# Kernel optimization log

Hardware: AMD Instinct MI355X
Metric: run time of the kernel (lower is better)

The kernel has to match this reference:

```python
import jax, jax.numpy as jnp
import numpy as np
from jax import lax

EMBED_DIM = 128
N_RELATIONS = 64
N_ENTITIES = 100000
N_EDGES = 600000


def setup_inputs() -> dict:
    key = jax.random.key(0)
    k1, k2, k3, k4, k5, k6 = jax.random.split(key, 6)
    entity_emb = jax.random.normal(k1, (N_ENTITIES, EMBED_DIM), dtype=jnp.float32)
    heads = jax.random.randint(k2, (N_EDGES,), 0, N_ENTITIES)
    rels = jax.random.randint(k3, (N_EDGES,), 0, N_RELATIONS)
    tails = jax.random.randint(k4, (N_EDGES,), 0, N_ENTITIES)
    # learned params: relation embedding table (std=0.01) and square Linear weight (xavier)
    rel_embed_weight = 0.01 * jax.random.normal(k5, (N_RELATIONS, EMBED_DIM), dtype=jnp.float32)
    xavier = float(np.sqrt(6.0 / (EMBED_DIM + EMBED_DIM)))
    W = jax.random.uniform(k6, (EMBED_DIM, EMBED_DIM), dtype=jnp.float32, minval=-xavier, maxval=xavier)
    return {"entity_emb": entity_emb, "rel_embed_weight": rel_embed_weight, "W": W,
            "heads": heads, "rels": rels, "tails": tails}


def reference(entity_emb, rel_embed_weight, W, heads, rels, tails):
    n_entities = entity_emb.shape[0]
    # gather edge endpoint / relation embeddings: [E, D]
    e_h = entity_emb[heads]
    e_t = entity_emb[tails]
    e_r = rel_embed_weight[rels]
    # tanh-gated dot-product score per edge: [E]
    score = jnp.sum(e_t * jnp.tanh(e_h + e_r), axis=-1)
    # global max-shift (detached in torch) then per-head segment softmax
    score_exp = jnp.exp(score - lax.stop_gradient(jnp.max(score)))
    score_sum = jax.ops.segment_sum(score_exp, heads, num_segments=n_entities)
    attn = score_exp / (score_sum[heads] + 1e-10)
    # scatter-add attention-weighted messages back to head nodes: [N, D]
    agg = jax.ops.segment_sum(attn[:, None] * e_t, heads, num_segments=n_entities)
    # final Linear (no bias) + LeakyReLU(0.2); dropout is identity in eval mode
    out = (entity_emb + agg) @ W.T
    return jax.nn.leaky_relu(out, negative_slope=0.2)
```

## Files before the change

### kernel.cpp

```cpp
#include <hip/hip_runtime.h>
#include <math.h>

#define EMBED 128
#define BMAX 8192
#define LDSPAD 136
#define DBINS 64

#define TWO_LOG2E 2.8853900817779268f
#define DEFER_THR 32.0f

#define TMASK 0xFFFFF

typedef __attribute__((ext_vector_type(8))) short short8;
typedef __attribute__((ext_vector_type(4))) float floatx4;

__device__ __forceinline__ float ex2(float x) { return __builtin_amdgcn_exp2f(x); }

__device__ __forceinline__ float fast_tanh2(float x) {
    float e = ex2(TWO_LOG2E * x);
    return 1.0f - 2.0f * __builtin_amdgcn_rcpf(1.0f + e);
}

__device__ __forceinline__ unsigned short f2b(float f) {
    union { float f; unsigned int u; } v; v.f = f;
    unsigned int r = v.u + 0x7FFFu + ((v.u >> 16) & 1u);
    return (unsigned short)(r >> 16);
}

__device__ __forceinline__ float b2f(short u) {
    union { float f; unsigned int i; } v;
    v.i = ((unsigned int)(unsigned short)u) << 16;
    return v.f;
}

template <int CTRL>
__device__ __forceinline__ float dpp_add_f(float x) {
    int y = __builtin_amdgcn_update_dpp(0, __float_as_int(x), CTRL, 0xF, 0xF, false);
    return x + __int_as_float(y);
}
__device__ __forceinline__ float dpp_sum16(float s) {
    s = dpp_add_f<0x121>(s);
    s = dpp_add_f<0x122>(s);
    s = dpp_add_f<0x124>(s);
    s = dpp_add_f<0x128>(s);
    return s;
}

__global__ __launch_bounds__(256) void k_cast_hist(
    const float* __restrict__ ent, const float* __restrict__ rel, const float* __restrict__ W,
    short* __restrict__ entb, short* __restrict__ relb, short* __restrict__ wb,
    const int* __restrict__ heads, int* __restrict__ cnt, int* __restrict__ ghist,
    int ngE, int ngR, int ngW, int E)
{
    if (blockIdx.x == 0 && threadIdx.x < DBINS) ghist[threadIdx.x] = 0;
    int stride = gridDim.x * 256;
    int total = ngE + ngR + ngW;
    for (int g = blockIdx.x * 256 + threadIdx.x; g < total; g += stride) {
        const float4* src; short* dst;
        if (g < ngE)            { src = (const float4*)ent + (size_t)g * 2;              dst = entb + (size_t)g * 8; }
        else if (g < ngE + ngR) { int g2 = g - ngE;       src = (const float4*)rel + (size_t)g2 * 2; dst = relb + (size_t)g2 * 8; }
        else                    { int g2 = g - ngE - ngR; src = (const float4*)W   + (size_t)g2 * 2; dst = wb   + (size_t)g2 * 8; }
        float4 a = src[0], b = src[1];
        short8 o;
        o[0] = (short)f2b(a.x); o[1] = (short)f2b(a.y); o[2] = (short)f2b(a.z); o[3] = (short)f2b(a.w);
        o[4] = (short)f2b(b.x); o[5] = (short)f2b(b.y); o[6] = (short)f2b(b.z); o[7] = (short)f2b(b.w);
        *(short8*)dst = o;
    }
    for (int e = blockIdx.x * 256 + threadIdx.x; e < E; e += stride)
        atomicAdd(cnt + heads[e], 1);
}

__global__ __launch_bounds__(1024) void k_scan1(
    const int* __restrict__ cnt, int* __restrict__ offs,
    int* __restrict__ bsum, int* __restrict__ ghist, int N)
{
    __shared__ int wsum[16];
    __shared__ int dh[DBINS];
    const int tid = threadIdx.x;
    if (tid < DBINS) dh[tid] = 0;
    int i = blockIdx.x * 1024 + tid;
    int v = (i < N) ? cnt[i] : 0;
    __syncthreads();
    if (i < N) atomicAdd(&dh[v < DBINS ? v : DBINS - 1], 1);
    int x = v;
    #pragma unroll
    for (int d = 1; d < 64; d <<= 1) {
        int y = __shfl_up(x, d, 64);
        if ((tid & 63) >= d) x += y;
    }
    if ((tid & 63) == 63) wsum[tid >> 6] = x;
    __syncthreads();
    if (tid < 16) {
        int w = wsum[tid];
        #pragma unroll
        for (int d = 1; d < 16; d <<= 1) {
            int y = __shfl_up(w, d, 16);
            if (tid >= d) w += y;
        }
        wsum[tid] = w;
    }
    __syncthreads();
    int add = (tid >= 64) ? wsum[(tid >> 6) - 1] : 0;
    int incl = x + add;
    if (i < N) offs[i] = incl - v;
    if (tid == 1023) bsum[blockIdx.x] = incl;
    if (tid < DBINS && dh[tid] > 0) atomicAdd(ghist + tid, dh[tid]);
}

__global__ __launch_bounds__(256) void k_scan23(
    int* __restrict__ offs, const int* __restrict__ bsum,
    int* __restrict__ cursor, const int* __restrict__ cnt,
    const int* __restrict__ ghist, int* __restrict__ bincur,
    int* __restrict__ order, int N, int nb)
{
    __shared__ int sb[256];
    __shared__ int ws4[4];
    __shared__ int dbs[DBINS];
    __shared__ int lcnt[DBINS];
    __shared__ int lbase[DBINS];
    const int tid = threadIdx.x;

    int v = (tid < nb) ? bsum[tid] : 0;
    int x = v;
    #pragma unroll
    for (int d = 1; d < 64; d <<= 1) {
        int y = __shfl_up(x, d, 64);
        if ((tid & 63) >= d) x += y;
    }
    if ((tid & 63) == 63) ws4[tid >> 6] = x;
    __syncthreads();
    if (tid < 4) {
        int w = ws4[tid];
        #pragma unroll
        for (int d = 1; d < 4; d <<= 1) {
            int y = __shfl_up(w, d, 4);
            if (tid >= d) w += y;
        }
        ws4[tid] = w;
    }
    __syncthreads();
    int add = (tid >= 64) ? ws4[(tid >> 6) - 1] : 0;
    sb[tid] = x + add - v;

    if (tid < 64) {
        int g = ghist[tid];
        int s = g;
        #pragma unroll
        for (int d = 1; d < 64; d <<= 1) {
            int y = __shfl_up(s, d, 64);
            if (tid >= d) s += y;
        }
        dbs[tid] = s - g;
    }
    if (tid < DBINS) lcnt[tid] = 0;
    __syncthreads();

    int i = blockIdx.x * 256 + tid;
    int deg = 0, lrank = 0;
    if (i < N) {
        int o = offs[i] + sb[i >> 10];
        offs[i] = o;
        cursor[i] = o;
        int c = cnt[i];
        deg = c < DBINS ? c : DBINS - 1;
        lrank = atomicAdd(&lcnt[deg], 1);
    }
    __syncthreads();
    if (tid < DBINS) {
        int n = lcnt[tid];
        lbase[tid] = (n > 0) ? (dbs[tid] + atomicAdd(bincur + tid, n)) : 0;
    }
    __syncthreads();
    if (i < N) order[lbase[deg] + lrank] = i;
}

__global__ __launch_bounds__(256) void k_csr(
    const int* __restrict__ heads, const int* __restrict__ rels,
    const int* __restrict__ tails, int* __restrict__ cursor,
    int* __restrict__ trp, int E)
{
    int e = blockIdx.x * 256 + threadIdx.x;
    if (e >= E) return;
    int pos = atomicAdd(cursor + heads[e], 1);
    trp[pos] = tails[e] | (rels[e] << 20);
}

__global__ __launch_bounds__(256) void k_fused(
    const short* __restrict__ entb, const short* __restrict__ relb,
    const int* __restrict__ offs, const int* __restrict__ cnt,
    const int* __restrict__ trp, const int* __restrict__ order,
    short* __restrict__ accb, float* __restrict__ mh, float* __restrict__ lh,
    float* __restrict__ blockmax, int N, int R)
{
    const int tid = threadIdx.x;
    const int lane = tid & 15;
    int head0 = blockIdx.x * 16 + (tid >> 4);
    int head  = (head0 < N) ? order[(N - 1) - head0] : N;
    float mt = -INFINITY;
    if (head < N) {
        int start = offs[head];
        int c     = cnt[head];
        short8 hh = *((const short8*)(entb + (size_t)head * EMBED) + lane);
        float hf[8];
        #pragma unroll
        for (int i = 0; i < 8; ++i) hf[i] = b2f(hh[i]);
        float m = -INFINITY;
        float l = 0.f;
        float acc[8] = {0,0,0,0,0,0,0,0};
        for (int base = 0; base < c; base += 16) {
            int rem = c - base;
            int mm  = rem < 16 ? rem : 16;
            int trv = 0;
            if (lane < mm) trv = trp[start + base + lane];
            int p0 = __shfl(trv, 0, 16);
            short8 vtc = *((const short8*)(entb + (size_t)(p0 & TMASK) * EMBED) + lane);
            short8 vrc = *((const short8*)(relb + (size_t)(p0 >> 20) * EMBED) + lane);
            for (int j = 0; j < mm; ++j) {
                int jn = (j + 1 < mm) ? j + 1 : j;
                int pn = __shfl(trv, jn, 16);
                short8 vtn = *((const short8*)(entb + (size_t)(pn & TMASK) * EMBED) + lane);
                short8 vrn = *((const short8*)(relb + (size_t)(pn >> 20) * EMBED) + lane);
                float s = 0.f;
                float vtf[8];
                #pragma unroll
                for (int i = 0; i < 8; ++i) {
                    vtf[i] = b2f(vtc[i]);
                    s = fmaf(vtf[i], fast_tanh2(hf[i] + b2f(vrc[i])), s);
                }
                s = dpp_sum16(s);
                mt = fmaxf(mt, s);
                float dlt = s - m;
                if (dlt > DEFER_THR) {
                    float alpha = __expf(-dlt);
                    l *= alpha;
                    #pragma unroll
                    for (int q = 0; q < 8; ++q) acc[q] *= alpha;
                    m = s;
                    dlt = 0.f;
                }
                float p = __expf(dlt);
                l += p;
                #pragma unroll
                for (int q = 0; q < 8; ++q)
                    acc[q] = fmaf(p, vtf[q], acc[q]);
                vtc = vtn;
                vrc = vrn;
            }
        }
        short8 o;
        #pragma unroll
        for (int q = 0; q < 8; ++q) o[q] = (short)f2b(acc[q]);
        *((short8*)(accb + (size_t)head * EMBED) + lane) = o;
        if (lane == 0) { mh[head] = m; lh[head] = l; }
    }
    __shared__ float wmax[4];
    float wm = mt;
    #pragma unroll
    for (int off = 1; off < 64; off <<= 1) wm = fmaxf(wm, __shfl_xor(wm, off, 64));
    if ((tid & 63) == 0) wmax[tid >> 6] = wm;
    __syncthreads();
    if (tid == 0)
        blockmax[blockIdx.x] = fmaxf(fmaxf(wmax[0], wmax[1]), fmaxf(wmax[2], wmax[3]));
}

__global__ __launch_bounds__(256) void k_maxred(
    const float* __restrict__ blockmax, float* __restrict__ Mout, int n)
{
    __shared__ float smax[256];
    float m = -INFINITY;
    for (int i = threadIdx.x; i < n; i += 256) m = fmaxf(m, blockmax[i]);
    smax[threadIdx.x] = m;
    __syncthreads();
    for (int off = 128; off > 0; off >>= 1) {
        if ((int)threadIdx.x < off)
            smax[threadIdx.x] = fmaxf(smax[threadIdx.x], smax[threadIdx.x + off]);
        __syncthreads();
    }
    if (threadIdx.x == 0) Mout[0] = smax[0];
}

__global__ __launch_bounds__(256) void k_gemm_f(
    const short* __restrict__ entb, const short* __restrict__ accb,
    const float* __restrict__ mh, const float* __restrict__ lh,
    const float* __restrict__ Mptr, const short* __restrict__ wb,
    float* __restrict__ out, int N)
{
    __shared__ short xs[128 * LDSPAD];
    __shared__ short ws[128 * LDSPAD];
    __shared__ float invs[128];
    const int tid = threadIdx.x;
    const int n0  = blockIdx.x * 128;
    const float M = Mptr[0];

    if (tid < 128) {
        int g = n0 + tid;
        invs[tid] = (g < N) ? 1.0f / (lh[g] + 1e-10f * __expf(M - mh[g])) : 0.f;
    }
    #pragma unroll
    for (int it = 0; it < 8; ++it) {
        int ch = it * 256 + tid;
        int row = ch >> 4, col8 = ch & 15;
        *(short8*)(ws + row * LDSPAD + col8 * 8) = ((const short8*)wb)[ch];
    }
    __syncthreads();
    #pragma unroll
    for (int it = 0; it < 8; ++it) {
        int ch = it * 256 + tid;
        int row = ch >> 4, col8 = ch & 15;
        int g = n0 + row;
        short8 v = {0,0,0,0,0,0,0,0};
        if (g < N) {
            float inv = invs[row];
            short8 e8 = *((const short8*)(entb + (size_t)g * EMBED) + col8);
            short8 a8 = *((const short8*)(accb + (size_t)g * EMBED) + col8);
            #pragma unroll
            for (int q = 0; q < 8; ++q)
                v[q] = (short)f2b(b2f(e8[q]) + b2f(a8[q]) * inv);
        }
        *(short8*)(xs + row * LDSPAD + col8 * 8) = v;
    }
    __syncthreads();

    const int wv   = tid >> 6;
    const int lane = tid & 63;
    const int n16  = lane & 15;
    const int quad = lane >> 4;

    floatx4 acc[2][8];
    #pragma unroll
    for (int rt = 0; rt < 2; ++rt)
        #pragma unroll
        for (int jt = 0; jt < 8; ++jt)
            acc[rt][jt] = (floatx4){0.f, 0.f, 0.f, 0.f};

    #pragma unroll
    for (int kc = 0; kc < 4; ++kc) {
        int koff = kc * 32 + quad * 8;
        short8 a0 = *(const short8*)(xs + (wv * 32      + n16) * LDSPAD + koff);
        short8 a1 = *(const short8*)(xs + (wv * 32 + 16 + n16) * LDSPAD + koff);
        #pragma unroll
        for (int jt = 0; jt < 8; ++jt) {
            short8 b = *(const short8*)(ws + (jt * 16 + n16) * LDSPAD + koff);
            acc[0][jt] = __builtin_amdgcn_mfma_f32_16x16x32_bf16(a0, b, acc[0][jt], 0, 0, 0);
            acc[1][jt] = __builtin_amdgcn_mfma_f32_16x16x32_bf16(a1, b, acc[1][jt], 0, 0, 0);
        }
    }

    #pragma unroll
    for (int rt = 0; rt < 2; ++rt) {
        int rowbase = n0 + wv * 32 + rt * 16 + quad * 4;
        #pragma unroll
        for (int r = 0; r < 4; ++r) {
            int grow = rowbase + r;
            if (grow < N) {
                float* o = out + (size_t)grow * EMBED + n16;
                #pragma unroll
                for (int jt = 0; jt < 8; ++jt) {
                    float v = acc[rt][jt][r];
                    o[jt * 16] = (v > 0.f) ? v : 0.2f * v;
                }
            }
        }
    }
}

extern "C" void kernel_launch(void* const* d_in, const int* in_sizes, int n_in,
                              void* d_out, int out_size, void* d_ws, size_t ws_size,
                              hipStream_t stream)
{
    const float* ent   = (const float*)d_in[0];
    const float* rel   = (const float*)d_in[1];
    const float* W     = (const float*)d_in[2];
    const int*   heads = (const int*)d_in[3];
    const int*   rels  = (const int*)d_in[4];
    const int*   tails = (const int*)d_in[5];
    const int E = in_sizes[3];
    const int N = in_sizes[0] / EMBED;
    const int R = in_sizes[1] / EMBED;
    float* out = (float*)d_out;

    short* accb     = (short*)d_ws;
    float* mh       = (float*)(accb + (size_t)N * EMBED);
    float* lh       = mh + N;
    int*   trp      = (int*)(lh + N);
    int*   cnt      = trp + E;
    int*   bincur   = cnt + N;
    int*   offs     = bincur + DBINS;
    int*   cursor   = offs + N;
    float* blockmax = (float*)(cursor + N);
    float* Mval     = blockmax + BMAX;
    int*   bsum     = (int*)(Mval + 4);
    int*   ghist    = bsum + 1024;
    int*   order    = ghist + DBINS;
    short* wb       = (short*)(order + N);
    short* entb     = wb + 16384;
    short* relb     = entb + (size_t)N * EMBED;

    const int nb  = (N + 1023) >> 10;
    const int ngh = (N + 15) / 16;

    hipMemsetAsync(cnt, 0, (size_t)(N + DBINS) * sizeof(int), stream);

    int ngE = N * EMBED / 8, ngR = R * EMBED / 8, ngW = EMBED * EMBED / 8;
    k_cast_hist<<<2048, 256, 0, stream>>>(ent, rel, W, entb, relb, wb, heads, cnt, ghist, ngE, ngR, ngW, E);
    k_scan1<<<nb, 1024, 0, stream>>>(cnt, offs, bsum, ghist, N);
    k_scan23<<<(N + 255) / 256, 256, 0, stream>>>(offs, bsum, cursor, cnt, ghist, bincur, order, N, nb);
    k_csr<<<(E + 255) / 256, 256, 0, stream>>>(heads, rels, tails, cursor, trp, E);
    k_fused<<<ngh, 256, 0, stream>>>(entb, relb, offs, cnt, trp, order, accb, mh, lh, blockmax, N, R);
    k_maxred<<<1, 256, 0, stream>>>(blockmax, Mval, ngh);
    k_gemm_f<<<(N + 127) / 128, 256, 0, stream>>>(entb, accb, mh, lh, Mval, wb, out, N);
}
```

Baseline: 242.9 us.

## Fold global max reduction into fused kernel and load GEMM A operand directly

Removes the separate single-block max-reduction kernel: each k_fused block atomically bumps a done counter, and the last block to finish reduces all block maxima and writes the global max. The counter is zeroed by extending the existing memset. In k_gemm_f, the X tile is no longer staged through LDS; each lane loads its entity and aggregate rows from global memory, combines them, and feeds them straight into the MFMA. This cuts LDS use and a barrier, at the cost of uncoalesced 16-byte global reads per lane and a serial tail in the last fused block.

After: 462.7 us. 90.5% more time.

```diff
diff --git a/kernel.cpp b/kernel.cpp
--- a/kernel.cpp
+++ b/kernel.cpp
@@ -190,7 +190,8 @@
     const int* __restrict__ offs, const int* __restrict__ cnt,
     const int* __restrict__ trp, const int* __restrict__ order,
     short* __restrict__ accb, float* __restrict__ mh, float* __restrict__ lh,
-    float* __restrict__ blockmax, int N, int R)
+    float* __restrict__ blockmax, unsigned int* __restrict__ done,
+    float* __restrict__ Mout, int N, int R)
 {
     const int tid = threadIdx.x;
     const int lane = tid & 15;
@@ -254,29 +255,31 @@
         if (lane == 0) { mh[head] = m; lh[head] = l; }
     }
     __shared__ float wmax[4];
+    __shared__ int lastflag;
     float wm = mt;
     #pragma unroll
     for (int off = 1; off < 64; off <<= 1) wm = fmaxf(wm, __shfl_xor(wm, off, 64));
     if ((tid & 63) == 0) wmax[tid >> 6] = wm;
     __syncthreads();
-    if (tid == 0)
+    if (tid == 0) {
         blockmax[blockIdx.x] = fmaxf(fmaxf(wmax[0], wmax[1]), fmaxf(wmax[2], wmax[3]));
-}
-
-__global__ __launch_bounds__(256) void k_maxred(
-    const float* __restrict__ blockmax, float* __restrict__ Mout, int n)
-{
-    __shared__ float smax[256];
-    float m = -INFINITY;
-    for (int i = threadIdx.x; i < n; i += 256) m = fmaxf(m, blockmax[i]);
-    smax[threadIdx.x] = m;
-    __syncthreads();
-    for (int off = 128; off > 0; off >>= 1) {
-        if ((int)threadIdx.x < off)
-            smax[threadIdx.x] = fmaxf(smax[threadIdx.x], smax[threadIdx.x + off]);
+        __threadfence();
+        unsigned int prev = atomicAdd(done, 1u);
+        lastflag = (prev == gridDim.x - 1) ? 1 : 0;
+    }
+    __syncthreads();
+    if (lastflag) {
+        __threadfence();
+        const volatile float* bm = (const volatile float*)blockmax;
+        float m2 = -INFINITY;
+        for (int i = tid; i < (int)gridDim.x; i += 256) m2 = fmaxf(m2, bm[i]);
+        #pragma unroll
+        for (int off = 1; off < 64; off <<= 1) m2 = fmaxf(m2, __shfl_xor(m2, off, 64));
+        if ((tid & 63) == 0) wmax[tid >> 6] = m2;
         __syncthreads();
-    }
-    if (threadIdx.x == 0) Mout[0] = smax[0];
+        if (tid == 0)
+            Mout[0] = fmaxf(fmaxf(wmax[0], wmax[1]), fmaxf(wmax[2], wmax[3]));
+    }
 }
 
 __global__ __launch_bounds__(256) void k_gemm_f(
@@ -285,7 +288,6 @@
     const float* __restrict__ Mptr, const short* __restrict__ wb,
     float* __restrict__ out, int N)
 {
-    __shared__ short xs[128 * LDSPAD];
     __shared__ short ws[128 * LDSPAD];
     __shared__ float invs[128];
     const int tid = threadIdx.x;
@@ -303,29 +305,17 @@
         *(short8*)(ws + row * LDSPAD + col8 * 8) = ((const short8*)wb)[ch];
     }
     __syncthreads();
-    #pragma unroll
-    for (int it = 0; it < 8; ++it) {
-        int ch = it * 256 + tid;
-        int row = ch >> 4, col8 = ch & 15;
-        int g = n0 + row;
-        short8 v = {0,0,0,0,0,0,0,0};
-        if (g < N) {
-            float inv = invs[row];
-            short8 e8 = *((const short8*)(entb + (size_t)g * EMBED) + col8);
-            short8 a8 = *((const short8*)(accb + (size_t)g * EMBED) + col8);
-            #pragma unroll
-            for (int q = 0; q < 8; ++q)
-                v[q] = (short)f2b(b2f(e8[q]) + b2f(a8[q]) * inv);
-        }
-        *(short8*)(xs + row * LDSPAD + col8 * 8) = v;
-    }
-    __syncthreads();
 
     const int wv   = tid >> 6;
     const int lane = tid & 63;
     const int n16  = lane & 15;
     const int quad = lane >> 4;
 
+    const int lr0 = wv * 32 + n16;
+    const int lr1 = lr0 + 16;
+    const int g0  = n0 + lr0;
+    const int g1  = n0 + lr1;
+
     floatx4 acc[2][8];
     #pragma unroll
     for (int rt = 0; rt < 2; ++rt)
@@ -333,11 +323,28 @@
         for (int jt = 0; jt < 8; ++jt)
             acc[rt][jt] = (floatx4){0.f, 0.f, 0.f, 0.f};
 
+    const float inv0 = invs[lr0];
+    const float inv1 = invs[lr1];
+
     #pragma unroll
     for (int kc = 0; kc < 4; ++kc) {
         int koff = kc * 32 + quad * 8;
-        short8 a0 = *(const short8*)(xs + (wv * 32      + n16) * LDSPAD + koff);
-        short8 a1 = *(const short8*)(xs + (wv * 32 + 16 + n16) * LDSPAD + koff);
+        short8 a0 = {0,0,0,0,0,0,0,0};
+        short8 a1 = {0,0,0,0,0,0,0,0};
+        if (g0 < N) {
+            short8 e8 = *(const short8*)(entb + (size_t)g0 * EMBED + koff);
+            short8 a8 = *(const short8*)(accb + (size_t)g0 * EMBED + koff);
+            #pragma unroll
+            for (int q = 0; q < 8; ++q)
+                a0[q] = (short)f2b(b2f(e8[q]) + b2f(a8[q]) * inv0);
+        }
+        if (g1 < N) {
+            short8 e8 = *(const short8*)(entb + (size_t)g1 * EMBED + koff);
+            short8 a8 = *(const short8*)(accb + (size_t)g1 * EMBED + koff);
+            #pragma unroll
+            for (int q = 0; q < 8; ++q)
+                a1[q] = (short)f2b(b2f(e8[q]) + b2f(a8[q]) * inv1);
+        }
         #pragma unroll
         for (int jt = 0; jt < 8; ++jt) {
             short8 b = *(const short8*)(ws + (jt * 16 + n16) * LDSPAD + koff);
@@ -385,7 +392,8 @@
     int*   trp      = (int*)(lh + N);
     int*   cnt      = trp + E;
     int*   bincur   = cnt + N;
-    int*   offs     = bincur + DBINS;
+    unsigned int* done = (unsigned int*)(bincur + DBINS);
+    int*   offs     = (int*)(done + 4);
     int*   cursor   = offs + N;
     float* blockmax = (float*)(cursor + N);
     float* Mval     = blockmax + BMAX;
@@ -399,14 +407,13 @@
     const int nb  = (N + 1023) >> 10;
     const int ngh = (N + 15) / 16;
 
-    hipMemsetAsync(cnt, 0, (size_t)(N + DBINS) * sizeof(int), stream);
+    hipMemsetAsync(cnt, 0, (size_t)(N + DBINS + 4) * sizeof(int), stream);
 
     int ngE = N * EMBED / 8, ngR = R * EMBED / 8, ngW = EMBED * EMBED / 8;
     k_cast_hist<<<2048, 256, 0, stream>>>(ent, rel, W, entb, relb, wb, heads, cnt, ghist, ngE, ngR, ngW, E);
     k_scan1<<<nb, 1024, 0, stream>>>(cnt, offs, bsum, ghist, N);
     k_scan23<<<(N + 255) / 256, 256, 0, stream>>>(offs, bsum, cursor, cnt, ghist, bincur, order, N, nb);
     k_csr<<<(E + 255) / 256, 256, 0, stream>>>(heads, rels, tails, cursor, trp, E);
-    k_fused<<<ngh, 256, 0, stream>>>(entb, relb, offs, cnt, trp, order, accb, mh, lh, blockmax, N, R);
-    k_maxred<<<1, 256, 0, stream>>>(blockmax, Mval, ngh);
+    k_fused<<<ngh, 256, 0, stream>>>(entb, relb, offs, cnt, trp, order, accb, mh, lh, blockmax, done, Mval, N, R);
     k_gemm_f<<<(N + 127) / 128, 256, 0, stream>>>(entb, accb, mh, lh, Mval, wb, out, N);
 }
```
